# Optimization experiments

Measured on AMD Instinct MI355X. Metric: run time of the kernel, lower is better.

Reference implementation:

```python
import jax, jax.numpy as jnp
import numpy as np

B, S, D, H = 4, 2048, 1024, 16
DH = D // H  # 64

def setup_inputs() -> dict:
    key = jax.random.key(0)
    k0, k1, k2, k3 = jax.random.split(key, 4)
    x = jax.random.normal(k0, (B, S, D), dtype=jnp.float32)
    # Linear layers use random_normal init, shape (D, D), no bias.
    Wq = jax.random.normal(k1, (D, D), dtype=jnp.float32) * 0.05
    Wk = jax.random.normal(k2, (D, D), dtype=jnp.float32) * 0.05
    Wv = jax.random.normal(k3, (D, D), dtype=jnp.float32) * 0.05
    return {"encoder_input": x, "Wq": Wq, "Wk": Wk, "Wv": Wv}

def reference(encoder_input, Wq, Wk, Wv):
    x = encoder_input
    n_heads = H
    # Per-document projections, batched: [B,S,D]
    q = jnp.einsum('bsd,de->bse', x, Wq)
    k = jnp.einsum('bsd,de->bse', x, Wk)
    v = jnp.einsum('bsd,de->bse', x, Wv)
    # np.split(..., H, axis=-1) == reshape last dim to [H, DH]
    q = q.reshape(B, S, n_heads, DH)
    k = k.reshape(B, S, n_heads, DH)
    v = v.reshape(B, S, n_heads, DH)
    # Scaled dot-product attention; NOTE: original divides by N_HEADS, not sqrt(d_head)
    scores = jnp.einsum('bqhd,bkhd->bhqk', q, k) / jnp.float32(n_heads)
    attn = jax.nn.softmax(scores, axis=-1)
    out = jnp.einsum('bhqk,bkhd->bqhd', attn, v)
    # Concatenate heads along last dim -> [B,S,D]
    return out.reshape(B, S, D)
```

## Files before the change

### kernel.cpp

```cpp
#include <hip/hip_runtime.h>

typedef unsigned short u16;
typedef unsigned int   u32;
typedef __bf16 bf16x8 __attribute__((ext_vector_type(8)));
typedef __bf16 bf16x4 __attribute__((ext_vector_type(4)));
typedef float  f32x4  __attribute__((ext_vector_type(4)));
typedef u32    u32x4  __attribute__((ext_vector_type(4)));
typedef u32    u32x2  __attribute__((ext_vector_type(2)));
typedef u16    u16x8  __attribute__((ext_vector_type(8)));

#define MFMA16(a,b,c) __builtin_amdgcn_mfma_f32_16x16x32_bf16(a,b,c,0,0,0)

#define BB 4
#define SS 2048
#define DD 1024
#define HH 16
#define DH 64
#define MM 8192

#define QSCALE 0.0901684400555602f

#define WAIT_VM0() __builtin_amdgcn_s_waitcnt(0x0F70)

__device__ __forceinline__ u16 f2bf(float f) {
  u32 u = __builtin_bit_cast(u32, f);
  u += 0x7fffu + ((u >> 16) & 1u);
  return (u16)(u >> 16);
}

__device__ __forceinline__ void async16(const void* g, void* l) {
  __builtin_amdgcn_global_load_lds(
      (const __attribute__((address_space(1))) unsigned int*)g,
      (__attribute__((address_space(3))) unsigned int*)l, 16, 0, 0);
}

__global__ __launch_bounds__(256) void convert_x(
    const float* __restrict__ in, u16* __restrict__ out)
{
  const size_t stride = (size_t)gridDim.x * 256 * 8;
  for (size_t i = ((size_t)blockIdx.x * 256 + threadIdx.x) * 8;
       i < (size_t)MM * DD; i += stride) {
    f32x4 a = *(const f32x4*)(in + i);
    f32x4 b = *(const f32x4*)(in + i + 4);
    u32x2 ua = __builtin_bit_cast(u32x2, __builtin_convertvector(a, bf16x4));
    u32x2 ub = __builtin_bit_cast(u32x2, __builtin_convertvector(b, bf16x4));
    u32x4 v = {ua[0], ua[1], ub[0], ub[1]};
    *(u32x4*)(out + i) = v;
  }
}

__global__ __launch_bounds__(256) void fill_sig(float* __restrict__ out, int n)
{
  for (int i = blockIdx.x * 256 + threadIdx.x; i < n; i += gridDim.x * 256)
    out[i] = 3.0f;
}

__global__ __launch_bounds__(256) void convert_w(
    const float* __restrict__ w0, const float* __restrict__ w1,
    const float* __restrict__ w2, u16* __restrict__ WtAll)
{
  const int z = blockIdx.z;
  const float* W = (z == 0) ? w0 : ((z == 1) ? w1 : w2);
  u16* Wt = WtAll + (size_t)z * DD * DD;
  const int n0 = blockIdx.x * 64;
  const int k0 = blockIdx.y * 64;
  __shared__ u16 tile[64][65];
#pragma unroll
  for (int i = 0; i < 16; ++i) {
    int e = threadIdx.x + i * 256;
    int r = e >> 6, c = e & 63;
    tile[r][c] = f2bf(W[(size_t)(k0 + r) * DD + n0 + c]);
  }
  __syncthreads();
#pragma unroll
  for (int i = 0; i < 16; ++i) {
    int e = threadIdx.x + i * 256;
    int r = e >> 6, c = e & 63;
    Wt[(size_t)(n0 + r) * DD + k0 + c] = tile[c][r];
  }
}

__global__ __launch_bounds__(256) void qkv_gemm(
    const u16* __restrict__ X, const u16* __restrict__ WtAll,
    u16* __restrict__ QKV)
{
  const int z = blockIdx.z;
  const u16* Wt = WtAll + (size_t)z * DD * DD;
  u16* Y = QKV + (size_t)z * MM * DD;
  const int m0 = blockIdx.x * 128;
  const int n0 = blockIdx.y * 128;
  const int t = threadIdx.x;
  const int ln = t & 63;
  const int w  = t >> 6;
  const int cl = ln & 15;
  const int qd = ln >> 4;
  const int wm = (w & 1) * 64;
  const int wn = (w >> 1) * 64;
  const int srow8   = ln >> 3;
  const int schunk8 = (ln & 7) * 8;

  __shared__ __align__(16) u16 Asm[128 * 64];
  __shared__ __align__(16) u16 Bsm[128 * 64];

  const f32x4 fzero = {0.f, 0.f, 0.f, 0.f};
  f32x4 acc[4][4];
#pragma unroll
  for (int i = 0; i < 4; ++i)
#pragma unroll
    for (int j = 0; j < 4; ++j) acc[i][j] = fzero;

  for (int k0 = 0; k0 < DD; k0 += 64) {
    __syncthreads();
#pragma unroll
    for (int c = 0; c < 4; ++c) {
      async16(X  + (size_t)(m0 + c * 32 + w * 8 + srow8) * DD + k0 + schunk8,
              Asm + (c * 32 + w * 8) * 64);
      async16(Wt + (size_t)(n0 + c * 32 + w * 8 + srow8) * DD + k0 + schunk8,
              Bsm + (c * 32 + w * 8) * 64);
    }
    WAIT_VM0();
    __syncthreads();

#pragma unroll
    for (int kk = 0; kk < 2; ++kk) {
      bf16x8 af[4], bf[4];
#pragma unroll
      for (int mb = 0; mb < 4; ++mb)
        af[mb] = *(const bf16x8*)&Asm[(wm + mb * 16 + cl) * 64 + kk * 32 + qd * 8];
#pragma unroll
      for (int nb = 0; nb < 4; ++nb)
        bf[nb] = *(const bf16x8*)&Bsm[(wn + nb * 16 + cl) * 64 + kk * 32 + qd * 8];
#pragma unroll
      for (int mb = 0; mb < 4; ++mb)
#pragma unroll
        for (int nb = 0; nb < 4; ++nb)
          acc[mb][nb] = MFMA16(af[mb], bf[nb], acc[mb][nb]);
    }
  }

  const float scl = (z == 0) ? QSCALE : 1.0f;
#pragma unroll
  for (int mb = 0; mb < 4; ++mb) {
#pragma unroll
    for (int r = 0; r < 4; ++r) {
      const size_t row = (size_t)(m0 + wm + mb * 16 + qd * 4 + r) * DD;
      f32x4 v = {acc[mb][0][r] * scl, acc[mb][1][r] * scl,
                 acc[mb][2][r] * scl, acc[mb][3][r] * scl};
      bf16x4 bv = __builtin_convertvector(v, bf16x4);
#pragma unroll
      for (int nb = 0; nb < 4; ++nb)
        *(__bf16*)&Y[row + n0 + wn + nb * 16 + cl] = bv[nb];
    }
  }
}

__global__ __launch_bounds__(256) void vtrans(
    const u16* __restrict__ V, u16* __restrict__ VtG)
{
  const int b = blockIdx.z;
  const int h = blockIdx.y;
  const int s0 = blockIdx.x * 64;
  __shared__ u16 tile[64][65];
#pragma unroll
  for (int i = 0; i < 16; ++i) {
    int e = threadIdx.x + i * 256;
    int r = e >> 6, c = e & 63;
    tile[r][c] = V[(size_t)(b * SS + s0 + r) * DD + h * DH + c];
  }
  __syncthreads();
#pragma unroll
  for (int i = 0; i < 16; ++i) {
    int e = threadIdx.x + i * 256;
    int r = e >> 6, c = e & 63;
    VtG[((size_t)(b * HH + h) * DH + r) * SS + s0 + c] = tile[c][r];
  }
}

__global__ __launch_bounds__(256, 2) void attn_kernel(
    const u16* __restrict__ QKV, const u16* __restrict__ VtG,
    float* __restrict__ Out)
{
  const int bh = blockIdx.x;
  const int b = bh >> 4;
  const int h = bh & 15;
  const int q0 = blockIdx.y * 256;
  const int t = threadIdx.x;
  const int ln = t & 63;
  const int w  = t >> 6;
  const int cl = ln & 15;
  const int qd = ln >> 4;
  const int srow = ln >> 2;
  const int swz = (((ln & 3) ^ ((srow >> 1) & 3)) << 3);
  const int sx = ((qd ^ ((cl >> 1) & 3)) << 3);

  const u16* Qg = QKV;
  const u16* Kg = QKV + (size_t)MM * DD;

  __shared__ __align__(16) u16 smem[20992];
  u16* const Pl = smem + 16384;

  const size_t qoff0 = (size_t)(b * SS + q0 + w * 16 + cl) * DD + h * DH;
  const bf16x8 qf0a = *(const bf16x8*)(Qg + qoff0 + qd * 8);
  const bf16x8 qf0b = *(const bf16x8*)(Qg + qoff0 + 32 + qd * 8);
  const bf16x8 qf1a = *(const bf16x8*)(Qg + qoff0 + (size_t)64 * DD + qd * 8);
  const bf16x8 qf1b = *(const bf16x8*)(Qg + qoff0 + (size_t)64 * DD + 32 + qd * 8);
  const bf16x8 qf2a = *(const bf16x8*)(Qg + qoff0 + (size_t)128 * DD + qd * 8);
  const bf16x8 qf2b = *(const bf16x8*)(Qg + qoff0 + (size_t)128 * DD + 32 + qd * 8);
  const bf16x8 qf3a = *(const bf16x8*)(Qg + qoff0 + (size_t)192 * DD + qd * 8);
  const bf16x8 qf3b = *(const bf16x8*)(Qg + qoff0 + (size_t)192 * DD + 32 + qd * 8);

  const f32x4 fzero = {0.f, 0.f, 0.f, 0.f};
  f32x4 oacc0[4], oacc1[4], oacc2[4], oacc3[4];
#pragma unroll
  for (int mt = 0; mt < 4; ++mt) {
    oacc0[mt] = fzero; oacc1[mt] = fzero; oacc2[mt] = fzero; oacc3[mt] = fzero;
  }
  float lsum0 = 0.f, lsum1 = 0.f, lsum2 = 0.f, lsum3 = 0.f;

  const size_t kgbase  = (size_t)b * SS * DD + (size_t)h * DH;
  const size_t vtgbase = ((size_t)(b * HH + h)) * DH * SS;

  u16* const Pw  = Pl + (w * 16 + cl) * 72;
  const u16* const Pr = Pl + (w * 16 + cl) * 72;

  auto stage = [&](int kt, int bi) {
    u16* kb = smem + bi * 4096;
    u16* vb = smem + 8192 + bi * 4096;
#pragma unroll
    for (int s = 0; s < 2; ++s) {
      async16(Kg  + kgbase + (size_t)(kt + w * 16 + srow) * DD + s * 32 + swz,
              kb + (s * 64 + w * 16) * 32);
      async16(VtG + vtgbase + (size_t)(w * 16 + srow) * SS + kt + s * 32 + swz,
              vb + (s * 64 + w * 16) * 32);
    }
  };

#define PAIR(QA0, QA1, QB0, QB1, OA, OB, LA, LB) do {                         \
    f32x4 stA[4], stB[4];                                                     \
    _Pragma("unroll")                                                         \
    for (int mt = 0; mt < 4; ++mt) {                                          \
      bf16x8 kf0 = *(const bf16x8*)&Kh[(mt * 16 + cl) * 32 + sx];             \
      bf16x8 kf1 = *(const bf16x8*)&Kh[(64 + mt * 16 + cl) * 32 + sx];        \
      f32x4 za = fzero, zb = fzero;                                           \
      za = MFMA16(kf0, QA0, za); za = MFMA16(kf1, QA1, za);                   \
      zb = MFMA16(kf0, QB0, zb); zb = MFMA16(kf1, QB1, zb);                   \
      stA[mt] = za; stB[mt] = zb;                                             \
    }                                                                         \
    _Pragma("unroll")                                                         \
    for (int mt = 0; mt < 4; ++mt) {                                          \
      f32x4 p;                                                                \
      _Pragma("unroll")                                                       \
      for (int r = 0; r < 4; ++r) {                                           \
        p[r] = __builtin_amdgcn_exp2f(stA[mt][r]);                            \
        LA += p[r];                                                           \
      }                                                                       \
      *(u32x2*)(Pw + mt * 16 + qd * 4) =                                      \
          __builtin_bit_cast(u32x2, __builtin_convertvector(p, bf16x4));      \
    }                                                                         \
    f32x4 pB[4];                                                              \
    _Pragma("unroll")                                                         \
    for (int mt = 0; mt < 4; ++mt) {                                          \
      _Pragma("unroll")                                                       \
      for (int r = 0; r < 4; ++r) {                                           \
        pB[mt][r] = __builtin_amdgcn_exp2f(stB[mt][r]);                       \
        LB += pB[mt][r];                                                      \
      }                                                                       \
    }                                                                         \
    {                                                                         \
      const bf16x8 pf0 = *(const bf16x8*)(Pr + qd * 8);                       \
      const bf16x8 pf1 = *(const bf16x8*)(Pr + 32 + qd * 8);                  \
      _Pragma("unroll")                                                       \
      for (int mt = 0; mt < 4; ++mt) {                                        \
        OA[mt] = MFMA16(vf0[mt], pf0, OA[mt]);                                \
        OA[mt] = MFMA16(vf1[mt], pf1, OA[mt]);                                \
      }                                                                       \
    }                                                                         \
    _Pragma("unroll")                                                         \
    for (int mt = 0; mt < 4; ++mt)                                            \
      *(u32x2*)(Pw + mt * 16 + qd * 4) =                                      \
          __builtin_bit_cast(u32x2, __builtin_convertvector(pB[mt], bf16x4)); \
    {                                                                         \
      const bf16x8 pf0 = *(const bf16x8*)(Pr + qd * 8);                       \
      const bf16x8 pf1 = *(const bf16x8*)(Pr + 32 + qd * 8);                  \
      _Pragma("unroll")                                                       \
      for (int mt = 0; mt < 4; ++mt) {                                        \
        OB[mt] = MFMA16(vf0[mt], pf0, OB[mt]);                                \
        OB[mt] = MFMA16(vf1[mt], pf1, OB[mt]);                                \
      }                                                                       \
    }                                                                         \
  } while (0)

  stage(0, 0);

  for (int it = 0; it < SS / 64; ++it) {
    const int cur = it & 1;
    WAIT_VM0();
    __syncthreads();
    if (it + 1 < SS / 64) stage((it + 1) * 64, cur ^ 1);

    const u16* Kh = smem + cur * 4096;
    const u16* Vh = smem + 8192 + cur * 4096;

    bf16x8 vf0[4], vf1[4];
#pragma unroll
    for (int mt = 0; mt < 4; ++mt) {
      vf0[mt] = *(const bf16x8*)&Vh[(mt * 16 + cl) * 32 + sx];
      vf1[mt] = *(const bf16x8*)&Vh[(64 + mt * 16 + cl) * 32 + sx];
    }

    PAIR(qf0a, qf0b, qf1a, qf1b, oacc0, oacc1, lsum0, lsum1);
    PAIR(qf2a, qf2b, qf3a, qf3b, oacc2, oacc3, lsum2, lsum3);
  }

  lsum0 += __shfl_xor(lsum0, 16); lsum0 += __shfl_xor(lsum0, 32);
  lsum1 += __shfl_xor(lsum1, 16); lsum1 += __shfl_xor(lsum1, 32);
  lsum2 += __shfl_xor(lsum2, 16); lsum2 += __shfl_xor(lsum2, 32);
  lsum3 += __shfl_xor(lsum3, 16); lsum3 += __shfl_xor(lsum3, 32);

  __syncthreads();
  float* Ol = (float*)smem;
  const int q   = ln >> 2;
  const int seg = ln & 3;
  const float* src = Ol + w * 1088 + q * 68 + seg * 16;

#define EPI(OA, LS, SOFF) do {                                                \
    const float inv = 1.f / (LS);                                             \
    _Pragma("unroll")                                                         \
    for (int mt = 0; mt < 4; ++mt) {                                          \
      f32x4 vv = OA[mt];                                                      \
      _Pragma("unroll")                                                       \
      for (int r = 0; r < 4; ++r) vv[r] *= inv;                               \
      *(f32x4*)(Ol + w * 1088 + cl * 68 + mt * 16 + qd * 4) = vv;             \
    }                                                                         \
    {                                                                         \
      float* dst = Out + (size_t)(b * SS + q0 + (SOFF) + w * 16 + q) * DD     \
                       + h * DH + seg * 16;                                   \
      _Pragma("unroll")                                                       \
      for (int i = 0; i < 4; ++i)                                             \
        *(f32x4*)(dst + i * 4) = *(const f32x4*)(src + i * 4);                \
    }                                                                         \
  } while (0)

  EPI(oacc0, lsum0, 0);
  EPI(oacc1, lsum1, 64);
  EPI(oacc2, lsum2, 128);
  EPI(oacc3, lsum3, 192);

#undef EPI
#undef PAIR
}

extern "C" void kernel_launch(void* const* d_in, const int* in_sizes, int n_in,
                              void* d_out, int out_size, void* d_ws, size_t ws_size,
                              hipStream_t stream)
{
  const float* x  = (const float*)d_in[0];
  const float* wq = (const float*)d_in[1];
  const float* wk = (const float*)d_in[2];
  const float* wv = (const float*)d_in[3];
  float* out = (float*)d_out;

  const size_t need = ((size_t)MM * DD + 3 * (size_t)DD * DD +
                       3 * (size_t)MM * DD + (size_t)MM * DD) * sizeof(u16);
  if (ws_size < need) {
    fill_sig<<<1024, 256, 0, stream>>>(out, out_size);
    return;
  }

  u16* xs  = (u16*)d_ws;
  u16* wt  = xs + (size_t)MM * DD;
  u16* qkv = wt + (size_t)3 * DD * DD;
  u16* vtg = qkv + (size_t)3 * MM * DD;

  convert_x<<<2048, 256, 0, stream>>>(x, xs);
  convert_w<<<dim3(16, 16, 3), 256, 0, stream>>>(wq, wk, wv, wt);
  qkv_gemm<<<dim3(64, 8, 3), 256, 0, stream>>>(xs, wt, qkv);
  vtrans<<<dim3(32, HH, BB), 256, 0, stream>>>(qkv + (size_t)2 * MM * DD, vtg);
  attn_kernel<<<dim3(HH * BB, SS / 256, 1), 256, 0, stream>>>(qkv, vtg, out);
}
```

Baseline: 253.2 us.

## Keep softmax probabilities in registers via permuted V layout, swizzle GEMM LDS

The attention kernel no longer round-trips the exponentiated scores through shared memory. The V-transpose kernel now writes keys in a permuted order so that the register layout of the S accumulator directly matches the B-operand layout needed by the PV MFMA, and the P values are packed in registers with shufflevector. K fragments are hoisted and loaded once per tile alongside V, and the QKV GEMM gains an XOR swizzle on its LDS tiles to reduce bank conflicts. This removes the LDS writes and reads for P and lowers shared memory use, at the cost of more live registers and a nonstandard Vt layout that correctness depends on.

```diff
diff --git a/kernel.cpp b/kernel.cpp
--- a/kernel.cpp
+++ b/kernel.cpp
@@ -96,8 +96,9 @@
   const int qd = ln >> 4;
   const int wm = (w & 1) * 64;
   const int wn = (w >> 1) * 64;
-  const int srow8   = ln >> 3;
-  const int schunk8 = (ln & 7) * 8;
+  const int srow8 = ln >> 3;
+  const int sch   = (((ln & 7) ^ (srow8 & 7)) << 3);
+  const int ch0   = ((qd ^ (cl & 7)) << 3);
 
   __shared__ __align__(16) u16 Asm[128 * 64];
   __shared__ __align__(16) u16 Bsm[128 * 64];
@@ -113,9 +114,9 @@
     __syncthreads();
 #pragma unroll
     for (int c = 0; c < 4; ++c) {
-      async16(X  + (size_t)(m0 + c * 32 + w * 8 + srow8) * DD + k0 + schunk8,
+      async16(X  + (size_t)(m0 + c * 32 + w * 8 + srow8) * DD + k0 + sch,
               Asm + (c * 32 + w * 8) * 64);
-      async16(Wt + (size_t)(n0 + c * 32 + w * 8 + srow8) * DD + k0 + schunk8,
+      async16(Wt + (size_t)(n0 + c * 32 + w * 8 + srow8) * DD + k0 + sch,
               Bsm + (c * 32 + w * 8) * 64);
     }
     WAIT_VM0();
@@ -126,10 +127,10 @@
       bf16x8 af[4], bf[4];
 #pragma unroll
       for (int mb = 0; mb < 4; ++mb)
-        af[mb] = *(const bf16x8*)&Asm[(wm + mb * 16 + cl) * 64 + kk * 32 + qd * 8];
+        af[mb] = *(const bf16x8*)&Asm[(wm + mb * 16 + cl) * 64 + (ch0 ^ (kk << 5))];
 #pragma unroll
       for (int nb = 0; nb < 4; ++nb)
-        bf[nb] = *(const bf16x8*)&Bsm[(wn + nb * 16 + cl) * 64 + kk * 32 + qd * 8];
+        bf[nb] = *(const bf16x8*)&Bsm[(wn + nb * 16 + cl) * 64 + (ch0 ^ (kk << 5))];
 #pragma unroll
       for (int mb = 0; mb < 4; ++mb)
 #pragma unroll
@@ -172,7 +173,9 @@
   for (int i = 0; i < 16; ++i) {
     int e = threadIdx.x + i * 256;
     int r = e >> 6, c = e & 63;
-    VtG[((size_t)(b * HH + h) * DH + r) * SS + s0 + c] = tile[c][r];
+    int k = c & 31;
+    int pos = (c & 32) + ((k & 15) >> 2) * 8 + (k >> 4) * 4 + (k & 3);
+    VtG[((size_t)(b * HH + h) * DH + r) * SS + s0 + pos] = tile[c][r];
   }
 }
 
@@ -196,8 +199,7 @@
   const u16* Qg = QKV;
   const u16* Kg = QKV + (size_t)MM * DD;
 
-  __shared__ __align__(16) u16 smem[20992];
-  u16* const Pl = smem + 16384;
+  __shared__ __align__(16) u16 smem[16384];
 
   const size_t qoff0 = (size_t)(b * SS + q0 + w * 16 + cl) * DD + h * DH;
   const bf16x8 qf0a = *(const bf16x8*)(Qg + qoff0 + qd * 8);
@@ -220,9 +222,6 @@
   const size_t kgbase  = (size_t)b * SS * DD + (size_t)h * DH;
   const size_t vtgbase = ((size_t)(b * HH + h)) * DH * SS;
 
-  u16* const Pw  = Pl + (w * 16 + cl) * 72;
-  const u16* const Pr = Pl + (w * 16 + cl) * 72;
-
   auto stage = [&](int kt, int bi) {
     u16* kb = smem + bi * 4096;
     u16* vb = smem + 8192 + bi * 4096;
@@ -239,49 +238,47 @@
     f32x4 stA[4], stB[4];                                                     \
     _Pragma("unroll")                                                         \
     for (int mt = 0; mt < 4; ++mt) {                                          \
-      bf16x8 kf0 = *(const bf16x8*)&Kh[(mt * 16 + cl) * 32 + sx];             \
-      bf16x8 kf1 = *(const bf16x8*)&Kh[(64 + mt * 16 + cl) * 32 + sx];        \
       f32x4 za = fzero, zb = fzero;                                           \
-      za = MFMA16(kf0, QA0, za); za = MFMA16(kf1, QA1, za);                   \
-      zb = MFMA16(kf0, QB0, zb); zb = MFMA16(kf1, QB1, zb);                   \
+      za = MFMA16(kf0[mt], QA0, za); za = MFMA16(kf1[mt], QA1, za);           \
+      zb = MFMA16(kf0[mt], QB0, zb); zb = MFMA16(kf1[mt], QB1, zb);           \
       stA[mt] = za; stB[mt] = zb;                                             \
     }                                                                         \
+    f32x4 pa0, pa1, pa2, pa3;                                                 \
     _Pragma("unroll")                                                         \
-    for (int mt = 0; mt < 4; ++mt) {                                          \
-      f32x4 p;                                                                \
-      _Pragma("unroll")                                                       \
-      for (int r = 0; r < 4; ++r) {                                           \
-        p[r] = __builtin_amdgcn_exp2f(stA[mt][r]);                            \
-        LA += p[r];                                                           \
-      }                                                                       \
-      *(u32x2*)(Pw + mt * 16 + qd * 4) =                                      \
-          __builtin_bit_cast(u32x2, __builtin_convertvector(p, bf16x4));      \
-    }                                                                         \
-    f32x4 pB[4];                                                              \
-    _Pragma("unroll")                                                         \
-    for (int mt = 0; mt < 4; ++mt) {                                          \
-      _Pragma("unroll")                                                       \
-      for (int r = 0; r < 4; ++r) {                                           \
-        pB[mt][r] = __builtin_amdgcn_exp2f(stB[mt][r]);                       \
-        LB += pB[mt][r];                                                      \
-      }                                                                       \
+    for (int r = 0; r < 4; ++r) {                                             \
+      pa0[r] = __builtin_amdgcn_exp2f(stA[0][r]); LA += pa0[r];               \
+      pa1[r] = __builtin_amdgcn_exp2f(stA[1][r]); LA += pa1[r];               \
+      pa2[r] = __builtin_amdgcn_exp2f(stA[2][r]); LA += pa2[r];               \
+      pa3[r] = __builtin_amdgcn_exp2f(stA[3][r]); LA += pa3[r];               \
     }                                                                         \
     {                                                                         \
-      const bf16x8 pf0 = *(const bf16x8*)(Pr + qd * 8);                       \
-      const bf16x8 pf1 = *(const bf16x8*)(Pr + 32 + qd * 8);                  \
+      bf16x8 pf0 = __builtin_shufflevector(                                   \
+          __builtin_convertvector(pa0, bf16x4),                               \
+          __builtin_convertvector(pa1, bf16x4), 0, 1, 2, 3, 4, 5, 6, 7);      \
+      bf16x8 pf1 = __builtin_shufflevector(                                   \
+          __builtin_convertvector(pa2, bf16x4),                               \
+          __builtin_convertvector(pa3, bf16x4), 0, 1, 2, 3, 4, 5, 6, 7);      \
       _Pragma("unroll")                                                       \
       for (int mt = 0; mt < 4; ++mt) {                                        \
         OA[mt] = MFMA16(vf0[mt], pf0, OA[mt]);                                \
         OA[mt] = MFMA16(vf1[mt], pf1, OA[mt]);                                \
       }                                                                       \
     }                                                                         \
+    f32x4 pb0, pb1, pb2, pb3;                                                 \
     _Pragma("unroll")                                                         \
-    for (int mt = 0; mt < 4; ++mt)                                            \
-      *(u32x2*)(Pw + mt * 16 + qd * 4) =                                      \
-          __builtin_bit_cast(u32x2, __builtin_convertvector(pB[mt], bf16x4)); \
+    for (int r = 0; r < 4; ++r) {                                             \
+      pb0[r] = __builtin_amdgcn_exp2f(stB[0][r]); LB += pb0[r];               \
+      pb1[r] = __builtin_amdgcn_exp2f(stB[1][r]); LB += pb1[r];               \
+      pb2[r] = __builtin_amdgcn_exp2f(stB[2][r]); LB += pb2[r];               \
+      pb3[r] = __builtin_amdgcn_exp2f(stB[3][r]); LB += pb3[r];               \
+    }                                                                         \
     {                                                                         \
-      const bf16x8 pf0 = *(const bf16x8*)(Pr + qd * 8);                       \
-      const bf16x8 pf1 = *(const bf16x8*)(Pr + 32 + qd * 8);                  \
+      bf16x8 pf0 = __builtin_shufflevector(                                   \
+          __builtin_convertvector(pb0, bf16x4),                               \
+          __builtin_convertvector(pb1, bf16x4), 0, 1, 2, 3, 4, 5, 6, 7);      \
+      bf16x8 pf1 = __builtin_shufflevector(                                   \
+          __builtin_convertvector(pb2, bf16x4),                               \
+          __builtin_convertvector(pb3, bf16x4), 0, 1, 2, 3, 4, 5, 6, 7);      \
       _Pragma("unroll")                                                       \
       for (int mt = 0; mt < 4; ++mt) {                                        \
         OB[mt] = MFMA16(vf0[mt], pf0, OB[mt]);                                \
@@ -301,9 +298,11 @@
     const u16* Kh = smem + cur * 4096;
     const u16* Vh = smem + 8192 + cur * 4096;
 
-    bf16x8 vf0[4], vf1[4];
+    bf16x8 kf0[4], kf1[4], vf0[4], vf1[4];
 #pragma unroll
     for (int mt = 0; mt < 4; ++mt) {
+      kf0[mt] = *(const bf16x8*)&Kh[(mt * 16 + cl) * 32 + sx];
+      kf1[mt] = *(const bf16x8*)&Kh[(64 + mt * 16 + cl) * 32 + sx];
       vf0[mt] = *(const bf16x8*)&Vh[(mt * 16 + cl) * 32 + sx];
       vf1[mt] = *(const bf16x8*)&Vh[(64 + mt * 16 + cl) * 32 + sx];
     }
```

Result: faster. 228.8 us (-9.6%).
